# Kernel tuning notes

Measured on AMD Instinct MI355X. Metric: run time of the kernel, lower is better.

The kernel has to match this reference:

```python
import jax, jax.numpy as jnp
import numpy as np
import math

DIM = 2048
D_STATE = 64
EXPAND = 2
CHUNK = 64
HEADDIM = 64
D_CONV = 4
D_INNER = EXPAND * DIM          # 4096
NHEADS = D_INNER // HEADDIM     # 64


def _segsum(x):
    """x: (..., T) -> (..., T, T); out[i,j] = sum_{k=j+1}^{i} x[k] for i>=j else -inf."""
    T = x.shape[-1]
    keep = jnp.tril(jnp.ones((T, T), bool), -1)          # strictly lower
    seg = jnp.cumsum(jnp.where(keep, x[..., None], 0.0), axis=-2)
    valid = jnp.tril(jnp.ones((T, T), bool))
    return jnp.where(valid, seg, -jnp.inf)


def _ssd(X, A, B, C, block):
    """Chunkwise SSD scan (Mamba-2 Listing 1). X:(b,L,h,p) A:(b,L,h) B,C:(b,L,h,n)."""
    b, L, h, p = X.shape
    n = B.shape[-1]
    c = L // block
    X = X.reshape(b, c, block, h, p)
    A = A.reshape(b, c, block, h)
    B = B.reshape(b, c, block, h, n)
    C = C.reshape(b, c, block, h, n)
    A = jnp.transpose(A, (0, 3, 1, 2))                    # (b,h,c,l)
    A_cum = jnp.cumsum(A, axis=-1)
    # intra-chunk (diagonal block) output
    L_intra = jnp.exp(_segsum(A))                         # (b,h,c,l,s)
    Y_diag = jnp.einsum('bclhn,bcshn,bhcls,bcshp->bclhp', C, B, L_intra, X)
    # per-chunk final states
    decay_states = jnp.exp(A_cum[..., -1:] - A_cum)       # (b,h,c,l)
    states = jnp.einsum('bclhn,bhcl,bclhp->bchpn', B, decay_states, X)
    states = jnp.concatenate([jnp.zeros_like(states[:, :1]), states], axis=1)
    # inter-chunk recurrence across chunk boundaries
    chunk_end = jnp.pad(A_cum[..., -1], ((0, 0), (0, 0), (1, 0)))  # (b,h,c+1)
    decay_chunk = jnp.exp(_segsum(chunk_end))             # (b,h,c+1,c+1)
    new_states = jnp.einsum('bhzc,bchpn->bzhpn', decay_chunk, states)
    states_per_chunk = new_states[:, :-1]
    # off-diagonal contribution from carried-in states
    state_decay_out = jnp.exp(A_cum)                      # (b,h,c,l)
    Y_off = jnp.einsum('bclhn,bchpn,bhcl->bclhp', C, states_per_chunk, state_decay_out)
    return (Y_diag + Y_off).reshape(b, L, h, p)


def setup_inputs() -> dict:
    key = jax.random.key(0)
    ks = jax.random.split(key, 6)
    b, l = 2, 2048
    x = jax.random.normal(ks[0], (b, l, DIM), jnp.float32)
    proj_out = 2 * D_INNER + 2 * D_STATE + NHEADS
    in_proj_w = jax.random.normal(ks[1], (proj_out, DIM), jnp.float32) / math.sqrt(DIM)
    conv_w = jax.random.normal(ks[2], (D_INNER, 1, D_CONV), jnp.float32) / math.sqrt(D_CONV)
    conv_b = jnp.zeros((D_INNER,), jnp.float32)
    out_proj_w = jax.random.normal(ks[3], (DIM, D_INNER), jnp.float32) / math.sqrt(D_INNER)
    A_log = jnp.zeros((NHEADS,), jnp.float32)
    D_skip = jnp.ones((D_INNER,), jnp.float32)
    u = jax.random.uniform(ks[4], (NHEADS,), jnp.float32)
    dt = jnp.clip(jnp.exp(u * (math.log(0.1) - math.log(0.001)) + math.log(0.001)), 1e-4, None)
    dt_bias = dt + jnp.log(-jnp.expm1(-dt))
    return dict(x=x, in_proj_w=in_proj_w, conv_w=conv_w, conv_b=conv_b,
                out_proj_w=out_proj_w, A_log=A_log, D_skip=D_skip, dt_bias=dt_bias)


def reference(x, in_proj_w, conv_w, conv_b, out_proj_w, A_log, D_skip, dt_bias):
    b, l, _ = x.shape
    proj = x @ in_proj_w.T
    splits = [D_INNER, 2 * D_INNER, 2 * D_INNER + D_STATE, 2 * D_INNER + 2 * D_STATE]
    x_branch, z, B_in, C_in, dt = jnp.split(proj, splits, axis=-1)
    # causal depthwise conv1d (torch pads both sides then slices [:l] == left-pad only)
    xc = jnp.transpose(x_branch, (0, 2, 1))               # (b, d_inner, l)
    xc = jax.lax.conv_general_dilated(
        xc, conv_w, (1,), [(D_CONV - 1, 0)],
        dimension_numbers=('NCH', 'OIH', 'NCH'), feature_group_count=D_INNER)
    xc = xc + conv_b[None, :, None]
    x_act = jax.nn.silu(jnp.transpose(xc, (0, 2, 1)))     # (b,l,d_inner)
    x_h = x_act.reshape(b, l, NHEADS, HEADDIM)
    dt_f = jax.nn.softplus(dt + dt_bias)                  # (b,l,h)
    A_f = -jnp.exp(A_log)                                 # (h,)
    X_disc = x_h * dt_f[..., None]
    A_disc = A_f[None, None, :] * dt_f
    B_b = jnp.broadcast_to(B_in[:, :, None, :], (b, l, NHEADS, D_STATE))
    C_b = jnp.broadcast_to(C_in[:, :, None, :], (b, l, NHEADS, D_STATE))
    Y = _ssd(X_disc, A_disc, B_b, C_b, CHUNK)             # (b,l,h,p)
    y = Y.reshape(b, l, D_INNER) + D_skip * x_act
    y = y * jax.nn.silu(z)
    return y @ out_proj_w.T
```

## Files before the change

kernel.cpp:

```cpp
#include <hip/hip_runtime.h>

typedef unsigned short u16;
typedef unsigned int   u32;
typedef __attribute__((ext_vector_type(8))) short bf16x8;
typedef __attribute__((ext_vector_type(4))) float f32x4;

__device__ __forceinline__ u16 f2bf(float f){
  u32 u = __builtin_bit_cast(u32, f);
  u32 r = (u + 0x7FFFu + ((u >> 16) & 1u)) >> 16;
  return (u16)r;
}
__device__ __forceinline__ float bf2f(u16 h){
  u32 u = ((u32)h) << 16;
  return __builtin_bit_cast(float, u);
}
__device__ __forceinline__ void llds16(const u16* g, u16* l){
  __builtin_amdgcn_global_load_lds((const __attribute__((address_space(1))) void*)g,
                                   (__attribute__((address_space(3))) void*)l, 16, 0, 0);
}

__global__ __launch_bounds__(256) void cast4(const float* __restrict__ in, u16* __restrict__ out, int n4){
  int i = blockIdx.x * 256 + threadIdx.x;
  if (i >= n4) return;
  float4 v = ((const float4*)in)[i];
  u32 lo = (u32)f2bf(v.x) | ((u32)f2bf(v.y) << 16);
  u32 hi = (u32)f2bf(v.z) | ((u32)f2bf(v.w) << 16);
  ((uint2*)out)[i] = make_uint2(lo, hi);
}

__global__ __launch_bounds__(256) void castpad_w1(const float* __restrict__ in, u16* __restrict__ out){
  int i = blockIdx.x * 256 + threadIdx.x;
  if (i >= 8448 * 512) return;
  int nrow = i >> 9;
  float4 v = make_float4(0.f, 0.f, 0.f, 0.f);
  if (nrow < 8384) v = ((const float4*)in)[i];
  u32 lo = (u32)f2bf(v.x) | ((u32)f2bf(v.y) << 16);
  u32 hi = (u32)f2bf(v.z) | ((u32)f2bf(v.w) << 16);
  ((uint2*)out)[i] = make_uint2(lo, hi);
}

template<bool OUTF32>
__global__ __launch_bounds__(256)
void gemm128(const u16* __restrict__ A, const u16* __restrict__ Bm, void* __restrict__ Cout,
             int NYT, int N, int K)
{
  __shared__ u16 As[8192], Bs[8192];
  const int tid = threadIdx.x;
  const int lane = tid & 63, wave = tid >> 6;
  const int wm = (wave >> 1) * 64, wn = (wave & 1) * 64;
  const int lr = lane & 15, lk8 = (lane >> 4) * 8;
  const int lterm = lr * 32 + (lk8 ^ ((lr & 8) << 1));
  const int nwg = gridDim.x;
  const int lid = blockIdx.x;
  const int q = nwg >> 3;
  const int swz = (lid & 7) * q + (lid >> 3);
  const int ty = swz % NYT, tx = swz / NYT;
  const size_t bm0 = (size_t)ty * 128;
  const size_t bn0 = (size_t)tx * 128;
  const int cg = (lane & 3) ^ ((lane & 32) ? 2 : 0);
  const int rsub = lane >> 2;
  const int ag0 = (wave >> 1) * 8;
  const int bg0 = (wave & 1) * 8;

  f32x4 acc[4][4] = {};

  for (int k0 = 0; k0 < K; k0 += 64) {
    __syncthreads();
    #pragma unroll
    for (int u = 0; u < 4; u++) {
      const int si = wave * 4 + u;
      const int row = (si >> 1) * 16 + rsub;
      const int kc = (si & 1) * 32 + cg * 8;
      llds16(A  + (bm0 + row) * (size_t)K + k0 + kc, As + si * 512 + lane * 8);
      llds16(Bm + (bn0 + row) * (size_t)K + k0 + kc, Bs + si * 512 + lane * 8);
    }
    __syncthreads();
    #pragma unroll
    for (int kb = 0; kb < 2; kb++) {
      bf16x8 af[4], bfv[4];
      #pragma unroll
      for (int m = 0; m < 4; m++) af[m]  = *(const bf16x8*)&As[(ag0 + m * 2 + kb) * 512 + lterm];
      #pragma unroll
      for (int n = 0; n < 4; n++) bfv[n] = *(const bf16x8*)&Bs[(bg0 + n * 2 + kb) * 512 + lterm];
      #pragma unroll
      for (int m = 0; m < 4; m++)
        #pragma unroll
        for (int n = 0; n < 4; n++)
          acc[m][n] = __builtin_amdgcn_mfma_f32_16x16x32_bf16(af[m], bfv[n], acc[m][n], 0, 0, 0);
    }
  }

  const int lg = (lane >> 4) * 4;
  #pragma unroll
  for (int m = 0; m < 4; m++)
    #pragma unroll
    for (int n = 0; n < 4; n++) {
      size_t col = bn0 + wn + n * 16 + lr;
      #pragma unroll
      for (int j = 0; j < 4; j++) {
        size_t row = bm0 + wm + m * 16 + lg + j;
        float v = acc[m][n][j];
        if (OUTF32) ((float*)Cout)[row * N + col] = v;
        else        ((u16*)Cout)[row * N + col] = f2bf(v);
      }
    }
}

__global__ __launch_bounds__(256)
void gemm128sk(const u16* __restrict__ A, const u16* __restrict__ Bm, float* __restrict__ P,
               int NYT, int N, int KLEN, int LDK)
{
  __shared__ u16 As[8192], Bs[8192];
  const int tid = threadIdx.x;
  const int lane = tid & 63, wave = tid >> 6;
  const int wm = (wave >> 1) * 64, wn = (wave & 1) * 64;
  const int lr = lane & 15, lk8 = (lane >> 4) * 8;
  const int lterm = lr * 32 + (lk8 ^ ((lr & 8) << 1));
  const int lid = blockIdx.x;
  const int ks = lid >> 9;
  const int lid2 = lid & 511;
  const int q = 512 >> 3;
  const int swz = (lid2 & 7) * q + (lid2 >> 3);
  const int ty = swz % NYT, tx = swz / NYT;
  const size_t bm0 = (size_t)ty * 128;
  const size_t bn0 = (size_t)tx * 128;
  const size_t koff = (size_t)ks * KLEN;
  float* Pout = P + (size_t)ks * 8388608;
  const int cg = (lane & 3) ^ ((lane & 32) ? 2 : 0);
  const int rsub = lane >> 2;
  const int ag0 = (wave >> 1) * 8;
  const int bg0 = (wave & 1) * 8;

  f32x4 acc[4][4] = {};

  for (int k0 = 0; k0 < KLEN; k0 += 64) {
    __syncthreads();
    #pragma unroll
    for (int u = 0; u < 4; u++) {
      const int si = wave * 4 + u;
      const int row = (si >> 1) * 16 + rsub;
      const int kc = (si & 1) * 32 + cg * 8;
      llds16(A  + (bm0 + row) * (size_t)LDK + koff + k0 + kc, As + si * 512 + lane * 8);
      llds16(Bm + (bn0 + row) * (size_t)LDK + koff + k0 + kc, Bs + si * 512 + lane * 8);
    }
    __syncthreads();
    #pragma unroll
    for (int kb = 0; kb < 2; kb++) {
      bf16x8 af[4], bfv[4];
      #pragma unroll
      for (int m = 0; m < 4; m++) af[m]  = *(const bf16x8*)&As[(ag0 + m * 2 + kb) * 512 + lterm];
      #pragma unroll
      for (int n = 0; n < 4; n++) bfv[n] = *(const bf16x8*)&Bs[(bg0 + n * 2 + kb) * 512 + lterm];
      #pragma unroll
      for (int m = 0; m < 4; m++)
        #pragma unroll
        for (int n = 0; n < 4; n++)
          acc[m][n] = __builtin_amdgcn_mfma_f32_16x16x32_bf16(af[m], bfv[n], acc[m][n], 0, 0, 0);
    }
  }

  const int lg = (lane >> 4) * 4;
  #pragma unroll
  for (int m = 0; m < 4; m++)
    #pragma unroll
    for (int n = 0; n < 4; n++) {
      size_t col = bn0 + wn + n * 16 + lr;
      #pragma unroll
      for (int j = 0; j < 4; j++) {
        size_t row = bm0 + wm + m * 16 + lg + j;
        Pout[row * N + col] = acc[m][n][j];
      }
    }
}

__global__ __launch_bounds__(256)
void addp(const float* __restrict__ p0, const float* __restrict__ p1, float* __restrict__ out){
  int i = blockIdx.x * 256 + threadIdx.x;
  float4 a = ((const float4*)p0)[i];
  float4 b = ((const float4*)p1)[i];
  ((float4*)out)[i] = make_float4(a.x + b.x, a.y + b.y, a.z + b.z, a.w + b.w);
}

__global__ __launch_bounds__(256)
void postproj(const u16* __restrict__ proj, const float* __restrict__ dt_bias,
              float* __restrict__ dtf, u16* __restrict__ Bb, u16* __restrict__ Cb)
{
  int i = blockIdx.x * 256 + threadIdx.x;
  if (i >= 4096 * 64) return;
  int bl = i >> 6, hh = i & 63;
  const u16* pr = proj + (size_t)bl * 8448;
  float dv = bf2f(pr[8320 + hh]) + dt_bias[hh];
  dtf[i] = dv > 20.f ? dv : log1pf(__expf(dv));
  Bb[i] = pr[8192 + hh];
  Cb[i] = pr[8256 + hh];
}

__global__ __launch_bounds__(256)
void conv_silu(const u16* __restrict__ proj, const float* __restrict__ cw,
               const float* __restrict__ cb, const float* __restrict__ dtf,
               u16* __restrict__ xact, u16* __restrict__ Xd)
{
  const int g = blockIdx.x;
  const int bl0 = g * 4;
  const int l0 = bl0 & 2047;
  const int d0 = blockIdx.y * 2048 + threadIdx.x * 8;
  const int hd = d0 >> 6;
  float4 wv[8];
  #pragma unroll
  for (int e = 0; e < 8; e++) wv[e] = *(const float4*)&cw[(size_t)(d0 + e) * 4];
  float bias[8];
  {
    float4 b0 = *(const float4*)&cb[d0];
    float4 b1 = *(const float4*)&cb[d0 + 4];
    bias[0]=b0.x; bias[1]=b0.y; bias[2]=b0.z; bias[3]=b0.w;
    bias[4]=b1.x; bias[5]=b1.y; bias[6]=b1.z; bias[7]=b1.w;
  }
  float r[7][8];
  #pragma unroll
  for (int t = 0; t < 7; t++) {
    const int l = l0 - 3 + t;
    if (l >= 0) {
      uint4 rv = *(const uint4*)(proj + (size_t)(bl0 - 3 + t) * 8448 + d0);
      const u16* re = (const u16*)&rv;
      #pragma unroll
      for (int e = 0; e < 8; e++) r[t][e] = bf2f(re[e]);
    } else {
      #pragma unroll
      for (int e = 0; e < 8; e++) r[t][e] = 0.f;
    }
  }
  #pragma unroll
  for (int lo = 0; lo < 4; lo++) {
    const float dt = dtf[(size_t)(bl0 + lo) * 64 + hd];
    u16 xo[8], xdo[8];
    #pragma unroll
    for (int e = 0; e < 8; e++) {
      float v = bias[e] + wv[e].x * r[lo][e] + wv[e].y * r[lo + 1][e]
                        + wv[e].z * r[lo + 2][e] + wv[e].w * r[lo + 3][e];
      float sil = v / (1.f + __expf(-v));
      xo[e]  = f2bf(sil);
      xdo[e] = f2bf(sil * dt);
    }
    *(uint4*)(xact + (size_t)(bl0 + lo) * 4096 + d0) = *(const uint4*)xo;
    *(uint4*)(Xd   + (size_t)(bl0 + lo) * 4096 + d0) = *(const uint4*)xdo;
  }
}

__global__ __launch_bounds__(256)
void ssd_states(const u16* __restrict__ Xd, const u16* __restrict__ Bg,
                const float* __restrict__ dtf, const float* __restrict__ A_log,
                u16* __restrict__ Stg, float* __restrict__ dtot)
{
  const int wg = blockIdx.x;
  const int b = wg >> 11, h = wg & 63;
  const int c = (wg >> 6) & 31;
  const int bl0 = b * 2048 + c * 64;
  __shared__ u16 Bt[64*64], Xts[64*64];
  __shared__ float avals[64], Acum[64], Adec[64];
  const int tid = threadIdx.x, wave = tid >> 6, lane = tid & 63;
  const int qi = (wave >> 1) * 32, qj = (wave & 1) * 32;
  const int lr = lane & 15, lk8 = (lane >> 4) * 8, lg = (lane >> 4) * 4;
  const float negA = -__expf(A_log[h]);

  if (tid < 64) avals[tid] = negA * dtf[(size_t)(bl0 + tid) * 64 + h];
  __syncthreads();
  if (tid < 64) { float s = 0.f; for (int j = 0; j <= tid; j++) s += avals[j]; Acum[tid] = s; }
  __syncthreads();
  if (tid < 64) Adec[tid] = __expf(Acum[63] - Acum[tid]);
  if (tid == 0) dtot[wg] = __expf(Acum[63]);
  __syncthreads();
  {
    int s = tid & 63, c0 = (tid >> 6) * 16;
    float dec = Adec[s];
    const u16* bs = Bg + (size_t)(bl0 + s) * 64 + c0;
    const u16* xs = Xd + (size_t)(bl0 + s) * 4096 + h * 64 + c0;
    #pragma unroll
    for (int j = 0; j < 16; j++) {
      Bt[(c0 + j) * 64 + s] = bs[j];
      Xts[(c0 + j) * 64 + s] = f2bf(bf2f(xs[j]) * dec);
    }
  }
  __syncthreads();
  f32x4 accst[2][2] = {};
  #pragma unroll
  for (int kk = 0; kk < 64; kk += 32) {
    bf16x8 xsf[2], btf[2];
    #pragma unroll
    for (int t = 0; t < 2; t++) {
      xsf[t] = *(const bf16x8*)&Xts[(qi + t * 16 + lr) * 64 + kk + lk8];
      btf[t] = *(const bf16x8*)&Bt [(qj + t * 16 + lr) * 64 + kk + lk8];
    }
    #pragma unroll
    for (int ti = 0; ti < 2; ti++)
      #pragma unroll
      for (int tj = 0; tj < 2; tj++)
        accst[ti][tj] = __builtin_amdgcn_mfma_f32_16x16x32_bf16(xsf[ti], btf[tj], accst[ti][tj], 0, 0, 0);
  }
  u16* So = Stg + (size_t)wg * 4096;
  #pragma unroll
  for (int ti = 0; ti < 2; ti++)
    #pragma unroll
    for (int tj = 0; tj < 2; tj++) {
      int nn = qj + tj * 16 + lr;
      #pragma unroll
      for (int r2 = 0; r2 < 4; r2++) {
        int pp = qi + ti * 16 + lg + r2;
        So[pp * 64 + nn] = f2bf(accst[ti][tj][r2]);
      }
    }
}

__global__ __launch_bounds__(256)
void ssd_scan(u16* __restrict__ Stg, const float* __restrict__ dtot)
{
  const int gid = blockIdx.x * 256 + threadIdx.x;
  const int bh = gid >> 12;
  const int pn = gid & 4095;
  const int b = bh >> 6, h = bh & 63;
  float R = 0.f;
  for (int c = 0; c < 32; ++c) {
    const int whc = b * 2048 + c * 64 + h;
    size_t idx = (size_t)whc * 4096 + pn;
    float st = bf2f(Stg[idx]);
    Stg[idx] = f2bf(R);
    R = R * dtot[whc] + st;
  }
}

__global__ __launch_bounds__(256)
void ssd_y(const u16* __restrict__ Xd, const u16* __restrict__ Bg, const u16* __restrict__ Cg,
           const float* __restrict__ dtf, const float* __restrict__ A_log,
           const u16* __restrict__ xact, const u16* __restrict__ proj,
           const float* __restrict__ Dskip, const u16* __restrict__ Stg,
           u16* __restrict__ Yout)
{
  const int wg = blockIdx.x;
  const int b = wg >> 11, h = wg & 63;
  const int c = (wg >> 6) & 31;
  const int bl0 = b * 2048 + c * 64;
  __shared__ u16 Cb[64*64], Bb[64*64], Xt[64*64], Sb[64*64], P[64*64];
  __shared__ float avals[64], Acum[64], Aexp[64];
  const int tid = threadIdx.x, wave = tid >> 6, lane = tid & 63;
  const int qi = (wave >> 1) * 32, qj = (wave & 1) * 32;
  const int lr = lane & 15, lk8 = (lane >> 4) * 8, lg = (lane >> 4) * 4;
  const float negA = -__expf(A_log[h]);

  if (tid < 64) avals[tid] = negA * dtf[(size_t)(bl0 + tid) * 64 + h];
  __syncthreads();
  if (tid < 64) { float s = 0.f; for (int j = 0; j <= tid; j++) s += avals[j]; Acum[tid] = s; }
  __syncthreads();
  if (tid < 64) Aexp[tid] = __expf(Acum[tid]);
  __syncthreads();
  {
    int l = tid >> 2, n0 = (tid & 3) * 16;
    const uint4* s0 = (const uint4*)(Cg + (size_t)(bl0 + l) * 64 + n0);
    *(uint4*)&Cb[l * 64 + n0] = s0[0]; *(uint4*)&Cb[l * 64 + n0 + 8] = s0[1];
    const uint4* s1 = (const uint4*)(Bg + (size_t)(bl0 + l) * 64 + n0);
    *(uint4*)&Bb[l * 64 + n0] = s1[0]; *(uint4*)&Bb[l * 64 + n0 + 8] = s1[1];
    int s = tid & 63, c0 = (tid >> 6) * 16;
    const u16* xs = Xd + (size_t)(bl0 + s) * 4096 + h * 64 + c0;
    #pragma unroll
    for (int j = 0; j < 16; j++) Xt[(c0 + j) * 64 + s] = xs[j];
    const uint4* sp = (const uint4*)(Stg + (size_t)wg * 4096 + tid * 16);
    *(uint4*)&Sb[tid * 16] = sp[0]; *(uint4*)&Sb[tid * 16 + 8] = sp[1];
  }
  __syncthreads();
  f32x4 accs[2][2] = {}; f32x4 accy[2][2] = {};
  #pragma unroll
  for (int kk = 0; kk < 64; kk += 32) {
    bf16x8 cf[2], bfr[2], sf[2];
    #pragma unroll
    for (int t = 0; t < 2; t++) {
      cf[t]  = *(const bf16x8*)&Cb[(qi + t * 16 + lr) * 64 + kk + lk8];
      bfr[t] = *(const bf16x8*)&Bb[(qj + t * 16 + lr) * 64 + kk + lk8];
      sf[t]  = *(const bf16x8*)&Sb[(qj + t * 16 + lr) * 64 + kk + lk8];
    }
    #pragma unroll
    for (int ti = 0; ti < 2; ti++)
      #pragma unroll
      for (int tj = 0; tj < 2; tj++) {
        accs[ti][tj] = __builtin_amdgcn_mfma_f32_16x16x32_bf16(cf[ti], bfr[tj], accs[ti][tj], 0, 0, 0);
        accy[ti][tj] = __builtin_amdgcn_mfma_f32_16x16x32_bf16(cf[ti], sf[tj],  accy[ti][tj], 0, 0, 0);
      }
  }
  #pragma unroll
  for (int ti = 0; ti < 2; ti++)
    #pragma unroll
    for (int tj = 0; tj < 2; tj++) {
      int j = qj + tj * 16 + lr;
      float Aj = Acum[j];
      #pragma unroll
      for (int r2 = 0; r2 < 4; r2++) {
        int i = qi + ti * 16 + lg + r2;
        float v = (i >= j) ? accs[ti][tj][r2] * __expf(Acum[i] - Aj) : 0.f;
        P[i * 64 + j] = f2bf(v);
        accy[ti][tj][r2] *= Aexp[i];
      }
    }
  __syncthreads();
  #pragma unroll
  for (int kk = 0; kk < 64; kk += 32) {
    bf16x8 pf[2], xf_[2];
    #pragma unroll
    for (int t = 0; t < 2; t++) {
      pf[t]  = *(const bf16x8*)&P [(qi + t * 16 + lr) * 64 + kk + lk8];
      xf_[t] = *(const bf16x8*)&Xt[(qj + t * 16 + lr) * 64 + kk + lk8];
    }
    #pragma unroll
    for (int ti = 0; ti < 2; ti++)
      #pragma unroll
      for (int tj = 0; tj < 2; tj++)
        accy[ti][tj] = __builtin_amdgcn_mfma_f32_16x16x32_bf16(pf[ti], xf_[tj], accy[ti][tj], 0, 0, 0);
  }
  #pragma unroll
  for (int ti = 0; ti < 2; ti++)
    #pragma unroll
    for (int tj = 0; tj < 2; tj++) {
      int pcol = qj + tj * 16 + lr;
      int d = h * 64 + pcol;
      float dsk = Dskip[d];
      #pragma unroll
      for (int r2 = 0; r2 < 4; r2++) {
        int lrow = qi + ti * 16 + lg + r2;
        size_t bl = (size_t)bl0 + lrow;
        float y = accy[ti][tj][r2];
        float xa = bf2f(xact[bl * 4096 + d]);
        float z = bf2f(proj[bl * 8448 + 4096 + d]);
        float sz = z / (1.f + __expf(-z));
        Yout[bl * 4096 + d] = f2bf((y + dsk * xa) * sz);
      }
    }
}

__global__ __launch_bounds__(256)
void ssd_kernel(const u16* __restrict__ Xd, const u16* __restrict__ Bg, const u16* __restrict__ Cg,
                const float* __restrict__ dtf, const float* __restrict__ A_log,
                const u16* __restrict__ xact, const u16* __restrict__ proj,
                const float* __restrict__ Dskip, u16* __restrict__ Yout)
{
  const int bh = blockIdx.x;
  const int b = bh >> 6, h = bh & 63;
  __shared__ float S[64 * 64];
  __shared__ u16 Cb[64*64], Bb[64*64], Bt[64*64], Xt[64*64], Xts[64*64], Sb[64*64], P[64*64];
  __shared__ float avals[64], Acum[64], Adec[64], Aexp[64];
  const int tid = threadIdx.x, wave = tid >> 6, lane = tid & 63;
  const int qi = (wave >> 1) * 32, qj = (wave & 1) * 32;
  const int lr = lane & 15, lk8 = (lane >> 4) * 8, lg = (lane >> 4) * 4;
  const float negA = -__expf(A_log[h]);

  for (int i = tid; i < 4096; i += 256) S[i] = 0.f;

  for (int c = 0; c < 32; ++c) {
    const int bl0 = b * 2048 + c * 64;
    __syncthreads();
    if (tid < 64) avals[tid] = negA * dtf[(size_t)(bl0 + tid) * 64 + h];
    __syncthreads();
    if (tid < 64) { float s = 0.f; for (int j = 0; j <= tid; j++) s += avals[j]; Acum[tid] = s; }
    __syncthreads();
    if (tid < 64) { float At = Acum[63]; Adec[tid] = __expf(At - Acum[tid]); Aexp[tid] = __expf(Acum[tid]); }
    __syncthreads();
    {
      int l = tid >> 2, n0 = (tid & 3) * 16;
      const uint4* s0 = (const uint4*)(Cg + (size_t)(bl0 + l) * 64 + n0);
      *(uint4*)&Cb[l * 64 + n0] = s0[0]; *(uint4*)&Cb[l * 64 + n0 + 8] = s0[1];
      const uint4* s1 = (const uint4*)(Bg + (size_t)(bl0 + l) * 64 + n0);
      *(uint4*)&Bb[l * 64 + n0] = s1[0]; *(uint4*)&Bb[l * 64 + n0 + 8] = s1[1];
      int s = tid & 63, c0 = (tid >> 6) * 16;
      float dec = Adec[s];
      const u16* bs = Bg + (size_t)(bl0 + s) * 64 + c0;
      const u16* xs = Xd + (size_t)(bl0 + s) * 4096 + h * 64 + c0;
      #pragma unroll
      for (int j = 0; j < 16; j++) {
        Bt[(c0 + j) * 64 + s] = bs[j];
        u16 xv = xs[j];
        Xt[(c0 + j) * 64 + s] = xv;
        Xts[(c0 + j) * 64 + s] = f2bf(bf2f(xv) * dec);
      }
      int p = tid >> 2, m0 = (tid & 3) * 16;
      #pragma unroll
      for (int j = 0; j < 16; j++) Sb[p * 64 + m0 + j] = f2bf(S[p * 64 + m0 + j]);
    }
    __syncthreads();
    f32x4 accs[2][2] = {}; f32x4 accy[2][2] = {};
    #pragma unroll
    for (int kk = 0; kk < 64; kk += 32) {
      bf16x8 cf[2], bfr[2], sf[2];
      #pragma unroll
      for (int t = 0; t < 2; t++) {
        cf[t]  = *(const bf16x8*)&Cb[(qi + t * 16 + lr) * 64 + kk + lk8];
        bfr[t] = *(const bf16x8*)&Bb[(qj + t * 16 + lr) * 64 + kk + lk8];
        sf[t]  = *(const bf16x8*)&Sb[(qj + t * 16 + lr) * 64 + kk + lk8];
      }
      #pragma unroll
      for (int ti = 0; ti < 2; ti++)
        #pragma unroll
        for (int tj = 0; tj < 2; tj++) {
          accs[ti][tj] = __builtin_amdgcn_mfma_f32_16x16x32_bf16(cf[ti], bfr[tj], accs[ti][tj], 0, 0, 0);
          accy[ti][tj] = __builtin_amdgcn_mfma_f32_16x16x32_bf16(cf[ti], sf[tj],  accy[ti][tj], 0, 0, 0);
        }
    }
    #pragma unroll
    for (int ti = 0; ti < 2; ti++)
      #pragma unroll
      for (int tj = 0; tj < 2; tj++) {
        int j = qj + tj * 16 + lr;
        float Aj = Acum[j];
        #pragma unroll
        for (int r2 = 0; r2 < 4; r2++) {
          int i = qi + ti * 16 + lg + r2;
          float v = (i >= j) ? accs[ti][tj][r2] * __expf(Acum[i] - Aj) : 0.f;
          P[i * 64 + j] = f2bf(v);
          accy[ti][tj][r2] *= Aexp[i];
        }
      }
    __syncthreads();
    f32x4 accst[2][2] = {};
    #pragma unroll
    for (int kk = 0; kk < 64; kk += 32) {
      bf16x8 pf[2], xf_[2], xsf[2], btf[2];
      #pragma unroll
      for (int t = 0; t < 2; t++) {
        pf[t]  = *(const bf16x8*)&P  [(qi + t * 16 + lr) * 64 + kk + lk8];
        xf_[t] = *(const bf16x8*)&Xt [(qj + t * 16 + lr) * 64 + kk + lk8];
        xsf[t] = *(const bf16x8*)&Xts[(qi + t * 16 + lr) * 64 + kk + lk8];
        btf[t] = *(const bf16x8*)&Bt [(qj + t * 16 + lr) * 64 + kk + lk8];
      }
      #pragma unroll
      for (int ti = 0; ti < 2; ti++)
        #pragma unroll
        for (int tj = 0; tj < 2; tj++) {
          accy[ti][tj]  = __builtin_amdgcn_mfma_f32_16x16x32_bf16(pf[ti],  xf_[tj], accy[ti][tj],  0, 0, 0);
          accst[ti][tj] = __builtin_amdgcn_mfma_f32_16x16x32_bf16(xsf[ti], btf[tj], accst[ti][tj], 0, 0, 0);
        }
    }
    float dtot = Aexp[63];
    #pragma unroll
    for (int ti = 0; ti < 2; ti++)
      #pragma unroll
      for (int tj = 0; tj < 2; tj++) {
        int nn = qj + tj * 16 + lr;
        #pragma unroll
        for (int r2 = 0; r2 < 4; r2++) {
          int pp = qi + ti * 16 + lg + r2;
          int idx = pp * 64 + nn;
          S[idx] = dtot * S[idx] + accst[ti][tj][r2];
        }
      }
    #pragma unroll
    for (int ti = 0; ti < 2; ti++)
      #pragma unroll
      for (int tj = 0; tj < 2; tj++) {
        int pcol = qj + tj * 16 + lr;
        int d = h * 64 + pcol;
        float dsk = Dskip[d];
        #pragma unroll
        for (int r2 = 0; r2 < 4; r2++) {
          int lrow = qi + ti * 16 + lg + r2;
          size_t bl = (size_t)bl0 + lrow;
          float y = accy[ti][tj][r2];
          float xa = bf2f(xact[bl * 4096 + d]);
          float z = bf2f(proj[bl * 8448 + 4096 + d]);
          float sz = z / (1.f + __expf(-z));
          Yout[bl * 4096 + d] = f2bf((y + dsk * xa) * sz);
        }
      }
  }
}

extern "C" void kernel_launch(void* const* d_in, const int* in_sizes, int n_in,
                              void* d_out, int out_size, void* d_ws, size_t ws_size,
                              hipStream_t stream) {
  const float* x    = (const float*)d_in[0];
  const float* w1   = (const float*)d_in[1];
  const float* cw   = (const float*)d_in[2];
  const float* cbv  = (const float*)d_in[3];
  const float* w2   = (const float*)d_in[4];
  const float* alog = (const float*)d_in[5];
  const float* dsk  = (const float*)d_in[6];
  const float* dtb  = (const float*)d_in[7];
  float* out = (float*)d_out;

  char* ws = (char*)d_ws;
  u16*  x_bf  = (u16*)(ws + 0);
  u16*  w1p   = (u16*)(ws + 16777216);
  u16*  w2b   = (u16*)(ws + 51380224);
  u16*  proj  = (u16*)(ws + 68157440);
  float* dtf  = (float*)(ws + 137363456);
  u16*  Bbf   = (u16*)(ws + 138412032);
  u16*  Cbf   = (u16*)(ws + 138936320);
  u16*  xact  = (u16*)(ws + 139460608);
  u16*  Xdd   = (u16*)(ws + 173015040);
  u16*  yin   = (u16*)(ws + 206569472);
  u16*  Stg   = (u16*)(ws + 240123904);
  float* dtot = (float*)(ws + 273678336);
  const size_t NEED_PAR = 273694720ull;
  float* p0 = (float*)(ws + 68157440);
  float* p1 = p0 + 8388608;

  cast4<<<8192, 256, 0, stream>>>(x,  x_bf, 2097152);
  castpad_w1<<<16896, 256, 0, stream>>>(w1, w1p);
  cast4<<<8192, 256, 0, stream>>>(w2, w2b, 2097152);

  gemm128<false><<<2112, 256, 0, stream>>>(x_bf, w1p, proj, 32, 8448, 2048);

  postproj<<<1024, 256, 0, stream>>>(proj, dtb, dtf, Bbf, Cbf);
  conv_silu<<<dim3(1024, 2), 256, 0, stream>>>(proj, cw, cbv, dtf, xact, Xdd);

  if (ws_size >= NEED_PAR) {
    ssd_states<<<4096, 256, 0, stream>>>(Xdd, Bbf, dtf, alog, Stg, dtot);
    ssd_scan<<<2048, 256, 0, stream>>>(Stg, dtot);
    ssd_y<<<4096, 256, 0, stream>>>(Xdd, Bbf, Cbf, dtf, alog, xact, proj, dsk, Stg, yin);
  } else {
    ssd_kernel<<<128, 256, 0, stream>>>(Xdd, Bbf, Cbf, dtf, alog, xact, proj, dsk, yin);
  }

  gemm128sk<<<1024, 256, 0, stream>>>(yin, w2b, p0, 32, 2048, 2048, 4096);
  addp<<<8192, 256, 0, stream>>>(p0, p1, out);
}
```

Before: 436.7 us.

## Merge cast kernels, drop Xd buffer, remap GEMM tiles per XCD

The three fp32-to-bf16 cast launches become a single kernel. conv_silu no longer writes the dt-scaled X copy; the SSD kernels instead scale x_act by dt when loading into LDS, which saves a 32MB write and its later reads. Both GEMMs replace the generic swizzle with a fixed XCD-aware tile mapping, so each XCD works on a compact block of output tiles for better L2 reuse. The fixed mapping hardcodes the problem shape, and the dt scaling now rounds from a different bf16 intermediate.

Measured after the change: 398.0 us. 1.1x faster.

```diff
diff --git a/kernel.cpp b/kernel.cpp
--- a/kernel.cpp
+++ b/kernel.cpp
@@ -19,30 +19,35 @@
                                    (__attribute__((address_space(3))) void*)l, 16, 0, 0);
 }
 
-__global__ __launch_bounds__(256) void cast4(const float* __restrict__ in, u16* __restrict__ out, int n4){
+__global__ __launch_bounds__(256)
+void castall(const float* __restrict__ x, const float* __restrict__ w1, const float* __restrict__ w2,
+             u16* __restrict__ x_bf, u16* __restrict__ w1p, u16* __restrict__ w2b)
+{
   int i = blockIdx.x * 256 + threadIdx.x;
-  if (i >= n4) return;
-  float4 v = ((const float4*)in)[i];
+  float4 v;
+  uint2* dst;
+  if (i < 2097152) {
+    v = ((const float4*)x)[i];
+    dst = (uint2*)x_bf + i;
+  } else if (i < 2097152 + 4325376) {
+    int j = i - 2097152;
+    int nrow = j >> 9;
+    v = make_float4(0.f, 0.f, 0.f, 0.f);
+    if (nrow < 8384) v = ((const float4*)w1)[j];
+    dst = (uint2*)w1p + j;
+  } else {
+    int j = i - 6422528;
+    v = ((const float4*)w2)[j];
+    dst = (uint2*)w2b + j;
+  }
   u32 lo = (u32)f2bf(v.x) | ((u32)f2bf(v.y) << 16);
   u32 hi = (u32)f2bf(v.z) | ((u32)f2bf(v.w) << 16);
-  ((uint2*)out)[i] = make_uint2(lo, hi);
-}
-
-__global__ __launch_bounds__(256) void castpad_w1(const float* __restrict__ in, u16* __restrict__ out){
-  int i = blockIdx.x * 256 + threadIdx.x;
-  if (i >= 8448 * 512) return;
-  int nrow = i >> 9;
-  float4 v = make_float4(0.f, 0.f, 0.f, 0.f);
-  if (nrow < 8384) v = ((const float4*)in)[i];
-  u32 lo = (u32)f2bf(v.x) | ((u32)f2bf(v.y) << 16);
-  u32 hi = (u32)f2bf(v.z) | ((u32)f2bf(v.w) << 16);
-  ((uint2*)out)[i] = make_uint2(lo, hi);
-}
-
-template<bool OUTF32>
-__global__ __launch_bounds__(256)
-void gemm128(const u16* __restrict__ A, const u16* __restrict__ Bm, void* __restrict__ Cout,
-             int NYT, int N, int K)
+  *dst = make_uint2(lo, hi);
+}
+
+__global__ __launch_bounds__(256)
+void gemm128(const u16* __restrict__ A, const u16* __restrict__ Bm, u16* __restrict__ Cout,
+             int N, int K)
 {
   __shared__ u16 As[8192], Bs[8192];
   const int tid = threadIdx.x;
@@ -50,11 +55,10 @@
   const int wm = (wave >> 1) * 64, wn = (wave & 1) * 64;
   const int lr = lane & 15, lk8 = (lane >> 4) * 8;
   const int lterm = lr * 32 + (lk8 ^ ((lr & 8) << 1));
-  const int nwg = gridDim.x;
   const int lid = blockIdx.x;
-  const int q = nwg >> 3;
-  const int swz = (lid & 7) * q + (lid >> 3);
-  const int ty = swz % NYT, tx = swz / NYT;
+  const int xcd = lid & 7, w = lid >> 3;
+  const int ty = (xcd & 3) * 8 + (w & 7);
+  const int tx = (xcd >> 2) * 33 + (w >> 3);
   const size_t bm0 = (size_t)ty * 128;
   const size_t bn0 = (size_t)tx * 128;
   const int cg = (lane & 3) ^ ((lane & 32) ? 2 : 0);
@@ -99,16 +103,14 @@
       #pragma unroll
       for (int j = 0; j < 4; j++) {
         size_t row = bm0 + wm + m * 16 + lg + j;
-        float v = acc[m][n][j];
-        if (OUTF32) ((float*)Cout)[row * N + col] = v;
-        else        ((u16*)Cout)[row * N + col] = f2bf(v);
+        Cout[row * N + col] = f2bf(acc[m][n][j]);
       }
     }
 }
 
 __global__ __launch_bounds__(256)
 void gemm128sk(const u16* __restrict__ A, const u16* __restrict__ Bm, float* __restrict__ P,
-               int NYT, int N, int KLEN, int LDK)
+               int N, int KLEN, int LDK)
 {
   __shared__ u16 As[8192], Bs[8192];
   const int tid = threadIdx.x;
@@ -119,9 +121,9 @@
   const int lid = blockIdx.x;
   const int ks = lid >> 9;
   const int lid2 = lid & 511;
-  const int q = 512 >> 3;
-  const int swz = (lid2 & 7) * q + (lid2 >> 3);
-  const int ty = swz % NYT, tx = swz / NYT;
+  const int xcd = lid2 & 7, w = lid2 >> 3;
+  const int ty = (xcd & 3) * 8 + (w & 7);
+  const int tx = (xcd >> 2) * 8 + (w >> 3);
   const size_t bm0 = (size_t)ty * 128;
   const size_t bn0 = (size_t)tx * 128;
   const size_t koff = (size_t)ks * KLEN;
@@ -197,14 +199,12 @@
 
 __global__ __launch_bounds__(256)
 void conv_silu(const u16* __restrict__ proj, const float* __restrict__ cw,
-               const float* __restrict__ cb, const float* __restrict__ dtf,
-               u16* __restrict__ xact, u16* __restrict__ Xd)
+               const float* __restrict__ cb, u16* __restrict__ xact)
 {
   const int g = blockIdx.x;
   const int bl0 = g * 4;
   const int l0 = bl0 & 2047;
   const int d0 = blockIdx.y * 2048 + threadIdx.x * 8;
-  const int hd = d0 >> 6;
   float4 wv[8];
   #pragma unroll
   for (int e = 0; e < 8; e++) wv[e] = *(const float4*)&cw[(size_t)(d0 + e) * 4];
@@ -231,23 +231,20 @@
   }
   #pragma unroll
   for (int lo = 0; lo < 4; lo++) {
-    const float dt = dtf[(size_t)(bl0 + lo) * 64 + hd];
-    u16 xo[8], xdo[8];
+    u16 xo[8];
     #pragma unroll
     for (int e = 0; e < 8; e++) {
       float v = bias[e] + wv[e].x * r[lo][e] + wv[e].y * r[lo + 1][e]
                         + wv[e].z * r[lo + 2][e] + wv[e].w * r[lo + 3][e];
       float sil = v / (1.f + __expf(-v));
       xo[e]  = f2bf(sil);
-      xdo[e] = f2bf(sil * dt);
     }
     *(uint4*)(xact + (size_t)(bl0 + lo) * 4096 + d0) = *(const uint4*)xo;
-    *(uint4*)(Xd   + (size_t)(bl0 + lo) * 4096 + d0) = *(const uint4*)xdo;
-  }
-}
-
-__global__ __launch_bounds__(256)
-void ssd_states(const u16* __restrict__ Xd, const u16* __restrict__ Bg,
+  }
+}
+
+__global__ __launch_bounds__(256)
+void ssd_states(const u16* __restrict__ xg, const u16* __restrict__ Bg,
                 const float* __restrict__ dtf, const float* __restrict__ A_log,
                 u16* __restrict__ Stg, float* __restrict__ dtot)
 {
@@ -271,13 +268,13 @@
   __syncthreads();
   {
     int s = tid & 63, c0 = (tid >> 6) * 16;
-    float dec = Adec[s];
+    float f = dtf[(size_t)(bl0 + s) * 64 + h] * Adec[s];
     const u16* bs = Bg + (size_t)(bl0 + s) * 64 + c0;
-    const u16* xs = Xd + (size_t)(bl0 + s) * 4096 + h * 64 + c0;
+    const u16* xs = xg + (size_t)(bl0 + s) * 4096 + h * 64 + c0;
     #pragma unroll
     for (int j = 0; j < 16; j++) {
       Bt[(c0 + j) * 64 + s] = bs[j];
-      Xts[(c0 + j) * 64 + s] = f2bf(bf2f(xs[j]) * dec);
+      Xts[(c0 + j) * 64 + s] = f2bf(bf2f(xs[j]) * f);
     }
   }
   __syncthreads();
@@ -328,11 +325,10 @@
 }
 
 __global__ __launch_bounds__(256)
-void ssd_y(const u16* __restrict__ Xd, const u16* __restrict__ Bg, const u16* __restrict__ Cg,
+void ssd_y(const u16* __restrict__ xg, const u16* __restrict__ Bg, const u16* __restrict__ Cg,
            const float* __restrict__ dtf, const float* __restrict__ A_log,
-           const u16* __restrict__ xact, const u16* __restrict__ proj,
-           const float* __restrict__ Dskip, const u16* __restrict__ Stg,
-           u16* __restrict__ Yout)
+           const u16* __restrict__ proj, const float* __restrict__ Dskip,
+           const u16* __restrict__ Stg, u16* __restrict__ Yout)
 {
   const int wg = blockIdx.x;
   const int b = wg >> 11, h = wg & 63;
@@ -358,9 +354,10 @@
     const uint4* s1 = (const uint4*)(Bg + (size_t)(bl0 + l) * 64 + n0);
     *(uint4*)&Bb[l * 64 + n0] = s1[0]; *(uint4*)&Bb[l * 64 + n0 + 8] = s1[1];
     int s = tid & 63, c0 = (tid >> 6) * 16;
-    const u16* xs = Xd + (size_t)(bl0 + s) * 4096 + h * 64 + c0;
-    #pragma unroll
-    for (int j = 0; j < 16; j++) Xt[(c0 + j) * 64 + s] = xs[j];
+    float dts = dtf[(size_t)(bl0 + s) * 64 + h];
+    const u16* xs = xg + (size_t)(bl0 + s) * 4096 + h * 64 + c0;
+    #pragma unroll
+    for (int j = 0; j < 16; j++) Xt[(c0 + j) * 64 + s] = f2bf(bf2f(xs[j]) * dts);
     const uint4* sp = (const uint4*)(Stg + (size_t)wg * 4096 + tid * 16);
     *(uint4*)&Sb[tid * 16] = sp[0]; *(uint4*)&Sb[tid * 16 + 8] = sp[1];
   }
@@ -424,7 +421,7 @@
         int lrow = qi + ti * 16 + lg + r2;
         size_t bl = (size_t)bl0 + lrow;
         float y = accy[ti][tj][r2];
-        float xa = bf2f(xact[bl * 4096 + d]);
+        float xa = bf2f(xg[bl * 4096 + d]);
         float z = bf2f(proj[bl * 8448 + 4096 + d]);
         float sz = z / (1.f + __expf(-z));
         Yout[bl * 4096 + d] = f2bf((y + dsk * xa) * sz);
@@ -433,10 +430,10 @@
 }
 
 __global__ __launch_bounds__(256)
-void ssd_kernel(const u16* __restrict__ Xd, const u16* __restrict__ Bg, const u16* __restrict__ Cg,
+void ssd_kernel(const u16* __restrict__ xg, const u16* __restrict__ Bg, const u16* __restrict__ Cg,
                 const float* __restrict__ dtf, const float* __restrict__ A_log,
-                const u16* __restrict__ xact, const u16* __restrict__ proj,
-                const float* __restrict__ Dskip, u16* __restrict__ Yout)
+                const u16* __restrict__ proj, const float* __restrict__ Dskip,
+                u16* __restrict__ Yout)
 {
   const int bh = blockIdx.x;
   const int b = bh >> 6, h = bh & 63;
@@ -467,14 +464,15 @@
       *(uint4*)&Bb[l * 64 + n0] = s1[0]; *(uint4*)&Bb[l * 64 + n0 + 8] = s1[1];
       int s = tid & 63, c0 = (tid >> 6) * 16;
       float dec = Adec[s];
+      float dts = dtf[(size_t)(bl0 + s) * 64 + h];
       const u16* bs = Bg + (size_t)(bl0 + s) * 64 + c0;
-      const u16* xs = Xd + (size_t)(bl0 + s) * 4096 + h * 64 + c0;
+      const u16* xs = xg + (size_t)(bl0 + s) * 4096 + h * 64 + c0;
       #pragma unroll
       for (int j = 0; j < 16; j++) {
         Bt[(c0 + j) * 64 + s] = bs[j];
-        u16 xv = xs[j];
-        Xt[(c0 + j) * 64 + s] = xv;
-        Xts[(c0 + j) * 64 + s] = f2bf(bf2f(xv) * dec);
+        float xv = bf2f(xs[j]) * dts;
+        Xt[(c0 + j) * 64 + s] = f2bf(xv);
+        Xts[(c0 + j) * 64 + s] = f2bf(xv * dec);
       }
       int p = tid >> 2, m0 = (tid & 3) * 16;
       #pragma unroll
@@ -558,7 +556,7 @@
           int lrow = qi + ti * 16 + lg + r2;
           size_t bl = (size_t)bl0 + lrow;
           float y = accy[ti][tj][r2];
-          float xa = bf2f(xact[bl * 4096 + d]);
+          float xa = bf2f(xg[bl * 4096 + d]);
           float z = bf2f(proj[bl * 8448 + 4096 + d]);
           float sz = z / (1.f + __expf(-z));
           Yout[bl * 4096 + d] = f2bf((y + dsk * xa) * sz);
@@ -589,7 +587,6 @@
   u16*  Bbf   = (u16*)(ws + 138412032);
   u16*  Cbf   = (u16*)(ws + 138936320);
   u16*  xact  = (u16*)(ws + 139460608);
-  u16*  Xdd   = (u16*)(ws + 173015040);
   u16*  yin   = (u16*)(ws + 206569472);
   u16*  Stg   = (u16*)(ws + 240123904);
   float* dtot = (float*)(ws + 273678336);
@@ -597,23 +594,21 @@
   float* p0 = (float*)(ws + 68157440);
   float* p1 = p0 + 8388608;
 
-  cast4<<<8192, 256, 0, stream>>>(x,  x_bf, 2097152);
-  castpad_w1<<<16896, 256, 0, stream>>>(w1, w1p);
-  cast4<<<8192, 256, 0, stream>>>(w2, w2b, 2097152);
-
-  gemm128<false><<<2112, 256, 0, stream>>>(x_bf, w1p, proj, 32, 8448, 2048);
+  castall<<<33280, 256, 0, stream>>>(x, w1, w2, x_bf, w1p, w2b);
+
+  gemm128<<<2112, 256, 0, stream>>>(x_bf, w1p, proj, 8448, 2048);
 
   postproj<<<1024, 256, 0, stream>>>(proj, dtb, dtf, Bbf, Cbf);
-  conv_silu<<<dim3(1024, 2), 256, 0, stream>>>(proj, cw, cbv, dtf, xact, Xdd);
+  conv_silu<<<dim3(1024, 2), 256, 0, stream>>>(proj, cw, cbv, xact);
 
   if (ws_size >= NEED_PAR) {
-    ssd_states<<<4096, 256, 0, stream>>>(Xdd, Bbf, dtf, alog, Stg, dtot);
+    ssd_states<<<4096, 256, 0, stream>>>(xact, Bbf, dtf, alog, Stg, dtot);
     ssd_scan<<<2048, 256, 0, stream>>>(Stg, dtot);
-    ssd_y<<<4096, 256, 0, stream>>>(Xdd, Bbf, Cbf, dtf, alog, xact, proj, dsk, Stg, yin);
+    ssd_y<<<4096, 256, 0, stream>>>(xact, Bbf, Cbf, dtf, alog, proj, dsk, Stg, yin);
   } else {
-    ssd_kernel<<<128, 256, 0, stream>>>(Xdd, Bbf, Cbf, dtf, alog, xact, proj, dsk, yin);
-  }
-
-  gemm128sk<<<1024, 256, 0, stream>>>(yin, w2b, p0, 32, 2048, 2048, 4096);
+    ssd_kernel<<<128, 256, 0, stream>>>(xact, Bbf, Cbf, dtf, alog, proj, dsk, yin);
+  }
+
+  gemm128sk<<<1024, 256, 0, stream>>>(yin, w2b, p0, 2048, 2048, 4096);
   addp<<<8192, 256, 0, stream>>>(p0, p1, out);
 }
```
